# Optimization experiments

Hardware: AMD Instinct MI355X
Metric: run time of the kernel (lower is better)

## Reference

```python
import jax, jax.numpy as jnp
import numpy as np

EPS = 0.001  # numerical_stabilizer


def setup_inputs() -> dict:
    key = jax.random.key(0)
    ks = jax.random.split(key, 8)
    B, L, D, H, M = 4, 4096, 1024, 16, 64
    scale = 0.02
    return {
        "query": jax.random.normal(ks[0], (B, L, D), jnp.float32),
        "key": jax.random.normal(ks[1], (B, L, D), jnp.float32),
        "value": jax.random.normal(ks[2], (B, L, D), jnp.float32),
        "Wq": jax.random.normal(ks[3], (D, H, M), jnp.float32) * scale,
        "bq": jnp.zeros((H, M), jnp.float32),
        "Wk": jax.random.normal(ks[4], (D, H, M), jnp.float32) * scale,
        "bk": jnp.zeros((H, M), jnp.float32),
        "Wv": jax.random.normal(ks[5], (D, H, M), jnp.float32) * scale,
        "bv": jnp.zeros((H, M), jnp.float32),
        "Wo": jax.random.normal(ks[6], (H, M, D), jnp.float32) * scale,
        "bo": jnp.zeros((D,), jnp.float32),
        "step": 0,
    }


def reference(query, key, value, Wq, bq, Wk, bk, Wv, bv, Wo, bo, step):
    # QKV projections: [B,L,D] x [D,H,M] -> [B,L,H,M]
    q = jnp.einsum('bld,dhm->blhm', query, Wq) + bq
    k = jnp.einsum('bld,dhm->blhm', key, Wk) + bk
    v = jnp.einsum('bld,dhm->blhm', value, Wv) + bv
    # ReLU feature map with stabilizer
    q = jax.nn.relu(q) + EPS
    k = jax.nn.relu(k) + EPS
    # Linear (kernelized) attention: KV outer-product state [B,H,M,M]
    kvs = jnp.einsum('blhm,blhd->bhmd', k, v)
    a_v = jnp.einsum('blhm,bhmd->blhd', q, kvs)
    # Normalizer: sum of keys over sequence
    ks_sum = jnp.sum(k, axis=1)                       # [B,H,M]
    norm = jnp.einsum('blhm,bhm->blh', q, ks_sum)     # [B,L,H]
    a_v = a_v / norm[..., None]
    # Output projection over (head, head_dim) -> hidden
    out = jnp.einsum('blhm,hmd->bld', a_v, Wo) + bo
    return out
```

## Files before the change

### kernel.cpp

```cpp
#include <hip/hip_runtime.h>
#include <stdint.h>


typedef __bf16 bf16;
typedef __bf16 bf16x4 __attribute__((ext_vector_type(4)));
typedef __bf16 bf16x8 __attribute__((ext_vector_type(8)));
typedef float f32x4 __attribute__((ext_vector_type(4)));

#define MFMA_(a, b, c) __builtin_amdgcn_mfma_f32_16x16x32_bf16((a), (b), (c), 0, 0, 0)

static constexpr int BB   = 4;
static constexpr int LSEQ = 4096;
static constexpr int DIM  = 1024;
static constexpr int HH   = 16;
static constexpr float EPSF = 0.001f;

__device__ __forceinline__ void gload16(bf16* lds, const bf16* g) {
  __builtin_amdgcn_global_load_lds(
      (const __attribute__((address_space(1))) void*)g,
      (__attribute__((address_space(3))) void*)lds, 16, 0, 0);
}

__device__ __forceinline__ void stage128(bf16* lds, const bf16* src, size_t ld,
                                         int wid, int lane) {
#pragma unroll
  for (int j = 0; j < 4; ++j) {
    const int chunk = wid * 4 + j;
    const int e = chunk * 512 + lane * 8;
    gload16(lds + chunk * 512, src + (size_t)(e >> 6) * ld + (e & 63));
  }
}

__global__ void k_cvt(const float* __restrict__ q, const float* __restrict__ k,
                      const float* __restrict__ v, bf16* __restrict__ xb) {
  const int which = blockIdx.y;
  const float* src = which == 0 ? q : (which == 1 ? k : v);
  bf16* dst = xb + (size_t)which * 16777216u;
  const size_t i = ((size_t)blockIdx.x * 256 + threadIdx.x) * 8;
  const float4 a = *reinterpret_cast<const float4*>(src + i);
  const float4 b = *reinterpret_cast<const float4*>(src + i + 4);
  bf16x8 o;
  o[0] = (bf16)a.x; o[1] = (bf16)a.y; o[2] = (bf16)a.z; o[3] = (bf16)a.w;
  o[4] = (bf16)b.x; o[5] = (bf16)b.y; o[6] = (bf16)b.z; o[7] = (bf16)b.w;
  *reinterpret_cast<bf16x8*>(dst + i) = o;
}

__global__ void k_prep_w4(const float* __restrict__ W0, const float* __restrict__ W1,
                          const float* __restrict__ W2, const float* __restrict__ W3,
                          bf16* __restrict__ T0, bf16* __restrict__ T1,
                          bf16* __restrict__ T2, bf16* __restrict__ T3) {
  const float* W; bf16* T;
  switch (blockIdx.z) {
    case 0:  W = W0; T = T0; break;
    case 1:  W = W1; T = T1; break;
    case 2:  W = W2; T = T2; break;
    default: W = W3; T = T3; break;
  }
  __shared__ float t[32][33];
  const int tx = threadIdx.x & 31, ty = threadIdx.x >> 5;
  const int r0 = blockIdx.x * 32, c0 = blockIdx.y * 32;
#pragma unroll
  for (int j = 0; j < 32; j += 8)
    t[ty + j][tx] = W[(size_t)(r0 + ty + j) * DIM + c0 + tx];
  __syncthreads();
#pragma unroll
  for (int j = 0; j < 32; j += 8)
    T[(size_t)(c0 + ty + j) * DIM + r0 + tx] = (bf16)t[tx][ty + j];
}

__global__ void k_init_vt(bf16* __restrict__ vt) {
  const int idx = blockIdx.x * 256 + threadIdx.x;
  const int l  = idx & (LSEQ - 1);
  const int r  = (idx >> 12) & 15;
  const int bh = idx >> 16;
  if (bh < BB * HH)
    vt[((size_t)bh * 80 + 64 + r) * LSEQ + l] = (r == 0) ? (bf16)1.0f : (bf16)0.0f;
}

template <int MODE>
__global__ void k_proj(const bf16* __restrict__ X, const bf16* __restrict__ WT,
                       const float* __restrict__ bias, bf16* __restrict__ out) {
  __shared__ bf16 As[128 * 64];
  __shared__ bf16 Bs[128 * 64];
  const int tid = threadIdx.x, lane = tid & 63, wid = tid >> 6;
  const int wr = wid >> 1, wc = wid & 1;
  const int lr = lane & 15, lk = lane >> 4;
  const int n0 = blockIdx.x * 128, c0 = blockIdx.y * 128;
  f32x4 acc[4][4] = {};

  for (int ks = 0; ks < 16; ++ks) {
    const int k0 = ks * 64;
    __syncthreads();
    stage128(As, X + (size_t)n0 * DIM + k0, DIM, wid, lane);
    stage128(Bs, WT + (size_t)c0 * DIM + k0, DIM, wid, lane);
    __syncthreads();
#pragma unroll
    for (int kk = 0; kk < 2; ++kk) {
      bf16x8 af[4], bfr[4];
#pragma unroll
      for (int rb = 0; rb < 4; ++rb)
        af[rb] = *reinterpret_cast<const bf16x8*>(&As[(wr * 64 + rb * 16 + lr) * 64 + kk * 32 + lk * 8]);
#pragma unroll
      for (int cb = 0; cb < 4; ++cb)
        bfr[cb] = *reinterpret_cast<const bf16x8*>(&Bs[(wc * 64 + cb * 16 + lr) * 64 + kk * 32 + lk * 8]);
#pragma unroll
      for (int rb = 0; rb < 4; ++rb)
#pragma unroll
        for (int cb = 0; cb < 4; ++cb)
          acc[rb][cb] = MFMA_(af[rb], bfr[cb], acc[rb][cb]);
    }
  }

  float bvv[4];
#pragma unroll
  for (int cb = 0; cb < 4; ++cb) bvv[cb] = bias[c0 + wc * 64 + cb * 16 + lr];
  const int bidx = n0 >> 12;
  const int l0 = n0 & (LSEQ - 1);
#pragma unroll
  for (int rb = 0; rb < 4; ++rb) {
#pragma unroll
    for (int cb = 0; cb < 4; ++cb) {
      const int c = c0 + wc * 64 + cb * 16 + lr;
      if (MODE == 0) {
#pragma unroll
        for (int r = 0; r < 4; ++r) {
          float x = acc[rb][cb][r] + bvv[cb];
          x = fmaxf(x, 0.f) + EPSF;
          const int row = n0 + wr * 64 + rb * 16 + lk * 4 + r;
          out[(size_t)row * DIM + c] = (bf16)x;
        }
      } else {
        const int l = l0 + wr * 64 + rb * 16 + lk * 4;
        bf16x4 o;
#pragma unroll
        for (int r = 0; r < 4; ++r) {
          float x = acc[rb][cb][r] + bvv[cb];
          if (MODE == 1) x = fmaxf(x, 0.f) + EPSF;
          o[r] = (bf16)x;
        }
        size_t rowbase;
        if (MODE == 1) rowbase = (size_t)bidx * 1024 + c;
        else           rowbase = ((size_t)(bidx * HH + (c >> 6)) * 80 + (c & 63));
        *reinterpret_cast<bf16x4*>(out + rowbase * LSEQ + l) = o;
      }
    }
  }
}

__global__ __launch_bounds__(256, 2) void k_kvs(const bf16* __restrict__ kt,
                                                const bf16* __restrict__ vt,
                                                float* __restrict__ kvs) {
  const int tid = threadIdx.x, lane = tid & 63, wid = tid >> 6;
  const int lr = lane & 15, lk = lane >> 4;
  const int bh = blockIdx.y;
  const int lbase = blockIdx.x * 1024;
  __shared__ bf16 As[64][64];
  __shared__ bf16 Bs[80][64];
  f32x4 acc[5] = {};
  const bf16* ktb = kt + (size_t)bh * 64 * LSEQ;
  const bf16* vtb = vt + (size_t)bh * 80 * LSEQ;

  for (int ks = 0; ks < 16; ++ks) {
    const int l0 = lbase + ks * 64;
    __syncthreads();
#pragma unroll
    for (int i = 0; i < 2; ++i) {
      const int e = i * 2048 + tid * 8;
      const int row = e >> 6, col = e & 63;
      *reinterpret_cast<bf16x8*>(&As[row][col]) =
          *reinterpret_cast<const bf16x8*>(ktb + (size_t)row * LSEQ + l0 + col);
    }
#pragma unroll
    for (int i = 0; i < 2; ++i) {
      const int e = i * 2048 + tid * 8;
      const int row = e >> 6, col = e & 63;
      *reinterpret_cast<bf16x8*>(&Bs[row][col]) =
          *reinterpret_cast<const bf16x8*>(vtb + (size_t)row * LSEQ + l0 + col);
    }
    if (tid < 128) {
      const int e = 4096 + tid * 8;
      const int row = e >> 6, col = e & 63;
      *reinterpret_cast<bf16x8*>(&Bs[row][col]) =
          *reinterpret_cast<const bf16x8*>(vtb + (size_t)row * LSEQ + l0 + col);
    }
    __syncthreads();
#pragma unroll
    for (int kk = 0; kk < 2; ++kk) {
      const bf16x8 af = *reinterpret_cast<const bf16x8*>(&As[wid * 16 + lr][kk * 32 + lk * 8]);
#pragma unroll
      for (int cb = 0; cb < 5; ++cb) {
        const bf16x8 bfr = *reinterpret_cast<const bf16x8*>(&Bs[cb * 16 + lr][kk * 32 + lk * 8]);
        acc[cb] = MFMA_(af, bfr, acc[cb]);
      }
    }
  }
  float* kb = kvs + (size_t)bh * 64 * 80;
#pragma unroll
  for (int cb = 0; cb < 5; ++cb) {
    const int dcol = cb * 16 + lr;
#pragma unroll
    for (int r = 0; r < 4; ++r) {
      const int m = wid * 16 + lk * 4 + r;
      atomicAdd(kb + m * 80 + dcol, acc[cb][r]);
    }
  }
}

__global__ void k_kvs_t(const float* __restrict__ kvs, bf16* __restrict__ bav) {
  const int bh = blockIdx.x;
  const float* src = kvs + (size_t)bh * 5120;
  bf16* dst = bav + (size_t)bh * 5120;
  for (int i = threadIdx.x; i < 5120; i += 256) {
    const int dp = i >> 6, mm = i & 63;
    dst[i] = (bf16)src[mm * 80 + dp];
  }
}

__global__ __launch_bounds__(256, 2) void k_av(const bf16* __restrict__ q,
                                               const bf16* __restrict__ bav,
                                               bf16* __restrict__ avn) {
  const int tid = threadIdx.x, lane = tid & 63, wid = tid >> 6;
  const int lr = lane & 15, lk = lane >> 4;
  const int bh = blockIdx.y, b = bh >> 4, h = bh & 15;
  const int l0 = blockIdx.x * 128;
  __shared__ bf16 As[128][64];
  __shared__ bf16 Bs[80][64];
  __shared__ float nrm[128];

  const bf16* qb = q + ((size_t)b * LSEQ + l0) * DIM + h * 64;
#pragma unroll
  for (int i = 0; i < 4; ++i) {
    const int e = i * 2048 + tid * 8;
    const int row = e >> 6, col = e & 63;
    *reinterpret_cast<bf16x8*>(&As[row][col]) =
        *reinterpret_cast<const bf16x8*>(qb + (size_t)row * DIM + col);
  }
  const bf16* bb = bav + (size_t)bh * 5120;
#pragma unroll
  for (int i = 0; i < 2; ++i) {
    const int e = i * 2048 + tid * 8;
    const int row = e >> 6, col = e & 63;
    *reinterpret_cast<bf16x8*>(&Bs[row][col]) =
        *reinterpret_cast<const bf16x8*>(bb + row * 64 + col);
  }
  if (tid < 128) {
    const int e = 4096 + tid * 8;
    const int row = e >> 6, col = e & 63;
    *reinterpret_cast<bf16x8*>(&Bs[row][col]) =
        *reinterpret_cast<const bf16x8*>(bb + row * 64 + col);
  }
  __syncthreads();

  f32x4 acc[2][5] = {};
#pragma unroll
  for (int kk = 0; kk < 2; ++kk) {
    bf16x8 af[2];
    af[0] = *reinterpret_cast<const bf16x8*>(&As[wid * 32 + lr][kk * 32 + lk * 8]);
    af[1] = *reinterpret_cast<const bf16x8*>(&As[wid * 32 + 16 + lr][kk * 32 + lk * 8]);
#pragma unroll
    for (int cb = 0; cb < 5; ++cb) {
      const bf16x8 bfr = *reinterpret_cast<const bf16x8*>(&Bs[cb * 16 + lr][kk * 32 + lk * 8]);
      acc[0][cb] = MFMA_(af[0], bfr, acc[0][cb]);
      acc[1][cb] = MFMA_(af[1], bfr, acc[1][cb]);
    }
  }
  if (lr == 0) {
#pragma unroll
    for (int rb = 0; rb < 2; ++rb)
#pragma unroll
      for (int r = 0; r < 4; ++r)
        nrm[wid * 32 + rb * 16 + lk * 4 + r] = acc[rb][4][r];
  }
  __syncthreads();
  bf16* ob = avn + ((size_t)b * LSEQ + l0) * DIM + h * 64;
#pragma unroll
  for (int rb = 0; rb < 2; ++rb) {
#pragma unroll
    for (int cb = 0; cb < 4; ++cb) {
#pragma unroll
      for (int r = 0; r < 4; ++r) {
        const int row = wid * 32 + rb * 16 + lk * 4 + r;
        const float x = acc[rb][cb][r] / nrm[row];
        ob[(size_t)row * DIM + cb * 16 + lr] = (bf16)x;
      }
    }
  }
}

__global__ void k_out(const bf16* __restrict__ A, const bf16* __restrict__ WoT,
                      const float* __restrict__ bo, float* __restrict__ out) {
  __shared__ bf16 As[128 * 64];
  __shared__ bf16 Bs[128 * 64];
  const int tid = threadIdx.x, lane = tid & 63, wid = tid >> 6;
  const int wr = wid >> 1, wc = wid & 1;
  const int lr = lane & 15, lk = lane >> 4;
  const int n0 = blockIdx.x * 128, c0 = blockIdx.y * 128;
  f32x4 acc[4][4] = {};

  for (int ks = 0; ks < 16; ++ks) {
    const int k0 = ks * 64;
    __syncthreads();
    stage128(As, A + (size_t)n0 * DIM + k0, DIM, wid, lane);
    stage128(Bs, WoT + (size_t)c0 * DIM + k0, DIM, wid, lane);
    __syncthreads();
#pragma unroll
    for (int kk = 0; kk < 2; ++kk) {
      bf16x8 af[4], bfr[4];
#pragma unroll
      for (int rb = 0; rb < 4; ++rb)
        af[rb] = *reinterpret_cast<const bf16x8*>(&As[(wr * 64 + rb * 16 + lr) * 64 + kk * 32 + lk * 8]);
#pragma unroll
      for (int cb = 0; cb < 4; ++cb)
        bfr[cb] = *reinterpret_cast<const bf16x8*>(&Bs[(wc * 64 + cb * 16 + lr) * 64 + kk * 32 + lk * 8]);
#pragma unroll
      for (int rb = 0; rb < 4; ++rb)
#pragma unroll
        for (int cb = 0; cb < 4; ++cb)
          acc[rb][cb] = MFMA_(af[rb], bfr[cb], acc[rb][cb]);
    }
  }
  float bvv[4];
#pragma unroll
  for (int cb = 0; cb < 4; ++cb) bvv[cb] = bo[c0 + wc * 64 + cb * 16 + lr];
#pragma unroll
  for (int rb = 0; rb < 4; ++rb)
#pragma unroll
    for (int cb = 0; cb < 4; ++cb)
#pragma unroll
      for (int r = 0; r < 4; ++r) {
        const int row = n0 + wr * 64 + rb * 16 + lk * 4 + r;
        const int c = c0 + wc * 64 + cb * 16 + lr;
        out[(size_t)row * DIM + c] = acc[rb][cb][r] + bvv[cb];
      }
}

extern "C" void kernel_launch(void* const* d_in, const int* in_sizes, int n_in,
                              void* d_out, int out_size, void* d_ws, size_t ws_size,
                              hipStream_t stream) {
  const float* query = (const float*)d_in[0];
  const float* key   = (const float*)d_in[1];
  const float* value = (const float*)d_in[2];
  const float* Wq    = (const float*)d_in[3];
  const float* bq    = (const float*)d_in[4];
  const float* Wk    = (const float*)d_in[5];
  const float* bk    = (const float*)d_in[6];
  const float* Wv    = (const float*)d_in[7];
  const float* bvp   = (const float*)d_in[8];
  const float* Wo    = (const float*)d_in[9];
  const float* bo    = (const float*)d_in[10];
  float* out = (float*)d_out;
  char* ws = (char*)d_ws;

  const size_t off_wqt = 0;
  const size_t off_wkt = off_wqt + (2u << 20);
  const size_t off_wvt = off_wkt + (2u << 20);
  const size_t off_wot = off_wvt + (2u << 20);
  const size_t off_xb  = off_wot + (2u << 20);
  const size_t off_vt  = off_xb  + 100663296ull;
  const size_t off_kvs = off_vt  + 41943040ull;
  const size_t off_bav = off_kvs + 1310720ull;
  const size_t total   = off_bav + 655360ull;
  if (ws_size < total) return;

  bf16*  WQT = (bf16*)(ws + off_wqt);
  bf16*  WKT = (bf16*)(ws + off_wkt);
  bf16*  WVT = (bf16*)(ws + off_wvt);
  bf16*  WOT = (bf16*)(ws + off_wot);
  bf16*  XB  = (bf16*)(ws + off_xb);
  bf16*  XBq = XB;
  bf16*  XBk = XB + 16777216u;
  bf16*  XBv = XB + 33554432u;
  bf16*  VT  = (bf16*)(ws + off_vt);
  float* KVS = (float*)(ws + off_kvs);
  bf16*  BAV = (bf16*)(ws + off_bav);
  bf16*  KT  = XBv;
  bf16*  Qb  = XBk;
  bf16*  AV  = XBq;

  k_cvt<<<dim3(8192, 3), 256, 0, stream>>>(query, key, value, XB);
  k_prep_w4<<<dim3(32, 32, 4), 256, 0, stream>>>(Wq, Wk, Wv, Wo, WQT, WKT, WVT, WOT);
  k_init_vt<<<16384, 256, 0, stream>>>(VT);
  hipMemsetAsync(KVS, 0, 1310720ull, stream);

  k_proj<2><<<dim3(128, 8), 256, 0, stream>>>(XBv, WVT, bvp, VT);
  k_proj<1><<<dim3(128, 8), 256, 0, stream>>>(XBk, WKT, bk, KT);
  k_proj<0><<<dim3(128, 8), 256, 0, stream>>>(XBq, WQT, bq, Qb);

  k_kvs<<<dim3(4, 64), 256, 0, stream>>>(KT, VT, KVS);
  k_kvs_t<<<64, 256, 0, stream>>>(KVS, BAV);

  k_av<<<dim3(32, 64), 256, 0, stream>>>(Qb, BAV, AV);

  k_out<<<dim3(128, 8), 256, 0, stream>>>(AV, WOT, bo, out);
}
```

Baseline: 284.6 us.

## Grid-stride nontemporal conversion, vectorized VT init, finer KV split

The fp32-to-bf16 conversion kernel becomes a grid-stride loop over fewer blocks and uses nontemporal loads, since the inputs are read only once. The VT constant-row initialization writes 8 bf16 values per thread instead of one, cutting the thread count. The KV-state reduction splits the sequence into 8 chunks instead of 4, doubling the block count for better occupancy at the cost of more atomic accumulation into KVS.

```diff
diff --git a/kernel.cpp b/kernel.cpp
--- a/kernel.cpp
+++ b/kernel.cpp
@@ -33,16 +33,20 @@
 
 __global__ void k_cvt(const float* __restrict__ q, const float* __restrict__ k,
                       const float* __restrict__ v, bf16* __restrict__ xb) {
-  const int which = blockIdx.y;
-  const float* src = which == 0 ? q : (which == 1 ? k : v);
-  bf16* dst = xb + (size_t)which * 16777216u;
-  const size_t i = ((size_t)blockIdx.x * 256 + threadIdx.x) * 8;
-  const float4 a = *reinterpret_cast<const float4*>(src + i);
-  const float4 b = *reinterpret_cast<const float4*>(src + i + 4);
-  bf16x8 o;
-  o[0] = (bf16)a.x; o[1] = (bf16)a.y; o[2] = (bf16)a.z; o[3] = (bf16)a.w;
-  o[4] = (bf16)b.x; o[5] = (bf16)b.y; o[6] = (bf16)b.z; o[7] = (bf16)b.w;
-  *reinterpret_cast<bf16x8*>(dst + i) = o;
+  const int nchunk = 3 << 21;
+  const int stride = gridDim.x * blockDim.x;
+  for (int c = blockIdx.x * blockDim.x + threadIdx.x; c < nchunk; c += stride) {
+    const int t = c >> 21;
+    const size_t off = (size_t)(c & ((1 << 21) - 1)) * 8;
+    const float* src = (t == 0) ? q : (t == 1) ? k : v;
+    const f32x4* sp = reinterpret_cast<const f32x4*>(src + off);
+    const f32x4 a = __builtin_nontemporal_load(sp);
+    const f32x4 b = __builtin_nontemporal_load(sp + 1);
+    bf16x8 o;
+    o[0] = (bf16)a[0]; o[1] = (bf16)a[1]; o[2] = (bf16)a[2]; o[3] = (bf16)a[3];
+    o[4] = (bf16)b[0]; o[5] = (bf16)b[1]; o[6] = (bf16)b[2]; o[7] = (bf16)b[3];
+    *reinterpret_cast<bf16x8*>(xb + (size_t)t * 16777216u + off) = o;
+  }
 }
 
 __global__ void k_prep_w4(const float* __restrict__ W0, const float* __restrict__ W1,
@@ -69,12 +73,15 @@
 }
 
 __global__ void k_init_vt(bf16* __restrict__ vt) {
-  const int idx = blockIdx.x * 256 + threadIdx.x;
-  const int l  = idx & (LSEQ - 1);
-  const int r  = (idx >> 12) & 15;
-  const int bh = idx >> 16;
-  if (bh < BB * HH)
-    vt[((size_t)bh * 80 + 64 + r) * LSEQ + l] = (r == 0) ? (bf16)1.0f : (bf16)0.0f;
+  const int c = blockIdx.x * 256 + threadIdx.x;
+  const int l8 = c & 511;
+  const int r  = (c >> 9) & 15;
+  const int bh = c >> 13;
+  const bf16 val = (r == 0) ? (bf16)1.0f : (bf16)0.0f;
+  bf16x8 o;
+#pragma unroll
+  for (int j = 0; j < 8; ++j) o[j] = val;
+  *reinterpret_cast<bf16x8*>(vt + ((size_t)bh * 80 + 64 + r) * LSEQ + l8 * 8) = o;
 }
 
 template <int MODE>
@@ -153,14 +160,14 @@
   const int tid = threadIdx.x, lane = tid & 63, wid = tid >> 6;
   const int lr = lane & 15, lk = lane >> 4;
   const int bh = blockIdx.y;
-  const int lbase = blockIdx.x * 1024;
+  const int lbase = blockIdx.x * 512;
   __shared__ bf16 As[64][64];
   __shared__ bf16 Bs[80][64];
   f32x4 acc[5] = {};
   const bf16* ktb = kt + (size_t)bh * 64 * LSEQ;
   const bf16* vtb = vt + (size_t)bh * 80 * LSEQ;
 
-  for (int ks = 0; ks < 16; ++ks) {
+  for (int ks = 0; ks < 8; ++ks) {
     const int l0 = lbase + ks * 64;
     __syncthreads();
 #pragma unroll
@@ -377,16 +384,16 @@
   bf16*  Qb  = XBk;
   bf16*  AV  = XBq;
 
-  k_cvt<<<dim3(8192, 3), 256, 0, stream>>>(query, key, value, XB);
+  k_cvt<<<2048, 256, 0, stream>>>(query, key, value, XB);
   k_prep_w4<<<dim3(32, 32, 4), 256, 0, stream>>>(Wq, Wk, Wv, Wo, WQT, WKT, WVT, WOT);
-  k_init_vt<<<16384, 256, 0, stream>>>(VT);
-  hipMemsetAsync(KVS, 0, 1310720ull, stream);
+  k_init_vt<<<2048, 256, 0, stream>>>(VT);
+  (void)hipMemsetAsync(KVS, 0, 1310720ull, stream);
 
   k_proj<2><<<dim3(128, 8), 256, 0, stream>>>(XBv, WVT, bvp, VT);
   k_proj<1><<<dim3(128, 8), 256, 0, stream>>>(XBk, WKT, bk, KT);
   k_proj<0><<<dim3(128, 8), 256, 0, stream>>>(XBq, WQT, bq, Qb);
 
-  k_kvs<<<dim3(4, 64), 256, 0, stream>>>(KT, VT, KVS);
+  k_kvs<<<dim3(8, 64), 256, 0, stream>>>(KT, VT, KVS);
   k_kvs_t<<<64, 256, 0, stream>>>(KVS, BAV);
 
   k_av<<<dim3(32, 64), 256, 0, stream>>>(Qb, BAV, AV);
```

Measured after the change: 280.2 us. No clear change (-1.5%).
